# Optimization experiments

Hardware: AMD Instinct MI355X
Metric: run time of the kernel (lower is better)

The kernel has to match this reference:

```python
import jax, jax.numpy as jnp
import numpy as np

B, S, D = 4, 2048, 1024
H, HD = 16, 64            # num heads, head dim (H*HD == D)
FF = 4096                  # llama intermediate size
EPS = 1e-6
THETA = 10000.0


def rms_norm(x, w):
    v = jnp.mean(jnp.square(x), axis=-1, keepdims=True)
    return x * jax.lax.rsqrt(v + EPS) * w


def apply_rope(x, pos):
    # x: [B,H,S,HD]; HF llama rotate_half convention
    inv = 1.0 / (THETA ** (jnp.arange(0, HD, 2, dtype=jnp.float32) / HD))  # [HD/2]
    ang = pos[:, None].astype(jnp.float32) * inv[None, :]                   # [S,HD/2]
    cos = jnp.concatenate([jnp.cos(ang), jnp.cos(ang)], -1)[None, None]     # [1,1,S,HD]
    sin = jnp.concatenate([jnp.sin(ang), jnp.sin(ang)], -1)[None, None]
    x1, x2 = jnp.split(x, 2, axis=-1)
    return x * cos + jnp.concatenate([-x2, x1], axis=-1) * sin


def setup_inputs() -> dict:
    key = jax.random.key(0)
    ks = jax.random.split(key, 12)
    p = lambda k, shp: (0.02 * jax.random.normal(k, shp, dtype=jnp.float32))
    return {
        "chunk_hidden_states": jax.random.normal(ks[0], (B, S, D), dtype=jnp.float32),
        "Wq": p(ks[1], (D, D)),
        "Wk": p(ks[2], (D, D)),
        "Wv": p(ks[3], (D, D)),
        "Wo": p(ks[4], (D, D)),
        "ln1_w": jnp.ones((D,), dtype=jnp.float32),
        "ln2_w": jnp.ones((D,), dtype=jnp.float32),
        "Wgate": p(ks[5], (FF, D)),
        "Wup": p(ks[6], (FF, D)),
        "Wdown": p(ks[7], (D, FF)),
        "W_out": p(ks[8], (1024, D)),
        "b_out": jnp.zeros((1024,), dtype=jnp.float32),
    }


def reference(chunk_hidden_states, Wq, Wk, Wv, Wo, ln1_w, ln2_w,
              Wgate, Wup, Wdown, W_out, b_out):
    x = chunk_hidden_states                      # [B,S,D]
    pos = jnp.arange(S)

    # --- self attention block ---
    h = rms_norm(x, ln1_w)
    q = (h @ Wq.T).reshape(B, S, H, HD).transpose(0, 2, 1, 3)  # [B,H,S,HD]
    k = (h @ Wk.T).reshape(B, S, H, HD).transpose(0, 2, 1, 3)
    v = (h @ Wv.T).reshape(B, S, H, HD).transpose(0, 2, 1, 3)
    q = apply_rope(q, pos)
    k = apply_rope(k, pos)
    # attention_mask is None when the layer is called directly -> full (non-causal) attention
    scores = jnp.einsum("bhqd,bhkd->bhqk", q, k) / jnp.sqrt(jnp.float32(HD))
    attn = jax.nn.softmax(scores, axis=-1)
    ctx = jnp.einsum("bhqk,bhkd->bhqd", attn, v)             # [B,H,S,HD]
    ctx = ctx.transpose(0, 2, 1, 3).reshape(B, S, D)
    x = x + ctx @ Wo.T

    # --- MLP block (SwiGLU) ---
    h2 = rms_norm(x, ln2_w)
    mlp = (jax.nn.silu(h2 @ Wgate.T) * (h2 @ Wup.T)) @ Wdown.T
    x = x + mlp

    # --- output head ---
    logits = x @ W_out.T + b_out                 # [B,S,1024]
    return logits.reshape(-1, 8, 1024)
```

## Files before the change

### kernel.cpp

```cpp
#include <hip/hip_runtime.h>

#define TB 4
#define TS 2048
#define TD 1024
#define TH 16
#define THD 64
#define TFF 4096
#define TTOK (TB*TS)

typedef unsigned int  uint32;
typedef unsigned short u16;
typedef short s8v __attribute__((ext_vector_type(8)));
typedef short s4bf __attribute__((ext_vector_type(4)));
typedef float f4v __attribute__((ext_vector_type(4)));

#define BF16_MAGIC 0x3f803f80u

__device__ __forceinline__ u16 f2bf(float f){
    uint32 u = __float_as_uint(f);
    u += 0x7fffu + ((u >> 16) & 1u);
    return (u16)(u >> 16);
}
__device__ __forceinline__ float bf2f(u16 h){
    return __uint_as_float(((uint32)h) << 16);
}
__device__ __forceinline__ void gload_lds16(const void* g, void* l){
    __builtin_amdgcn_global_load_lds(
        (const __attribute__((address_space(1))) unsigned int*)g,
        (__attribute__((address_space(3))) unsigned int*)l,
        16, 0, 0);
}

struct CvtDesc { const void* src; void* dst; int n; int mode; };
struct CvtArgs { CvtDesc d[13]; };

__global__ __launch_bounds__(256)
void cvt_all(CvtArgs a, const uint32* __restrict__ flag){
    const bool isbf = (*flag == BF16_MAGIC);
    CvtDesc dd = a.d[blockIdx.y];
    if (dd.mode == 2){
        float* cosT = (float*)dd.dst;
        float* sinT = cosT + TS*32;
        for (int i = blockIdx.x*256 + threadIdx.x; i < dd.n; i += 256*gridDim.x){
            int s = i >> 5, f = i & 31;
            double inv = pow(10000.0, -(double)f/32.0);
            double ang = (double)s * inv;
            cosT[i] = (float)cos(ang);
            sinT[i] = (float)sin(ang);
        }
        return;
    }
    int n4 = dd.n >> 2;
    if (dd.mode == 1){
        float* dst = (float*)dd.dst;
        for (int i = blockIdx.x*256 + threadIdx.x; i < n4; i += 256*gridDim.x){
            float4 v;
            if (isbf){
                ushort4 u = ((const ushort4*)dd.src)[i];
                v = make_float4(bf2f(u.x), bf2f(u.y), bf2f(u.z), bf2f(u.w));
            } else v = ((const float4*)dd.src)[i];
            ((float4*)dst)[i] = v;
        }
        return;
    }
    for (int i = blockIdx.x*256 + threadIdx.x; i < n4; i += 256*gridDim.x){
        ushort4 o;
        if (isbf) o = ((const ushort4*)dd.src)[i];
        else {
            float4 v = ((const float4*)dd.src)[i];
            o.x=f2bf(v.x); o.y=f2bf(v.y); o.z=f2bf(v.z); o.w=f2bf(v.w);
        }
        size_t di = i;
        if (dd.mode >= 3){
            int row = i >> 8, c4 = i & 255;
            int drow = ((row >> 6) << 7) + (row & 63) + ((dd.mode == 4) ? 64 : 0);
            di = (size_t)drow*256 + c4;
        }
        ((ushort4*)dd.dst)[di] = o;
    }
}

__global__ __launch_bounds__(256)
void rmsnorm_k(const float* __restrict__ x, const float* __restrict__ w, u16* __restrict__ out){
    int row = blockIdx.x, tid = threadIdx.x;
    float4 xv = ((const float4*)(x + (size_t)row*TD))[tid];
    float s = xv.x*xv.x + xv.y*xv.y + xv.z*xv.z + xv.w*xv.w;
    #pragma unroll
    for (int off = 32; off > 0; off >>= 1) s += __shfl_xor(s, off);
    __shared__ float red[4];
    if ((tid & 63) == 0) red[tid >> 6] = s;
    __syncthreads();
    float tot = red[0]+red[1]+red[2]+red[3];
    float rs = rsqrtf(tot * (1.0f/TD) + 1e-6f);
    float4 wv = ((const float4*)w)[tid];
    ushort4 o;
    o.x = f2bf(xv.x*rs*wv.x); o.y = f2bf(xv.y*rs*wv.y);
    o.z = f2bf(xv.z*rs*wv.z); o.w = f2bf(xv.w*rs*wv.w);
    ((ushort4*)(out + (size_t)row*TD))[tid] = o;
}

enum { EPI_ADDF32 = 1, EPI_OUT = 3, EPI_QKVROPE = 4, EPI_ADDBF16 = 5, EPI_GATEUP = 6 };

template<int EPI>
__global__ __launch_bounds__(256)
void gemm_bt(const u16* __restrict__ A, int lda,
             const u16* __restrict__ W, int ldw,
             int K,
             void* __restrict__ outp, int ldo,
             const float* __restrict__ bias,
             const uint32* __restrict__ flag,
             u16* __restrict__ q_out, u16* __restrict__ k_out, u16* __restrict__ vt_out,
             const float* __restrict__ cosT, const float* __restrict__ sinT,
             const float* __restrict__ resid)
{
    __shared__ __align__(16) u16 SMEM[2*128*64];
    u16* As = SMEM;
    u16* Bs = SMEM + 128*64;
    const int tid  = threadIdx.x;
    const int wave = tid >> 6;
    const int lane = tid & 63;
    const int tm = blockIdx.y * 128;
    const int tn = blockIdx.x * 128;
    const int wm = (wave >> 1) * 64;
    const int wn = (wave &  1) * 64;

    f4v acc[4][4] = {};

    const int srow8 = lane >> 3;
    const int ch    = lane & 7;
    const int lrow  = lane & 15;
    const int lq    = lane >> 4;

    const u16* Ag = A + (size_t)(tm + wave*32 + srow8)*lda + ((ch ^ srow8) << 3);
    const u16* Wg = W + (size_t)(tn + wave*32 + srow8)*ldw + ((ch ^ srow8) << 3);

    for (int k0 = 0; k0 < K; k0 += 64){
        __syncthreads();
        #pragma unroll
        for (int i8 = 0; i8 < 4; i8++){
            gload_lds16(Ag + (size_t)(i8*8)*lda + k0, As + (wave*32 + i8*8)*64);
            gload_lds16(Wg + (size_t)(i8*8)*ldw + k0, Bs + (wave*32 + i8*8)*64);
        }
        __syncthreads();

        #pragma unroll
        for (int kk = 0; kk < 2; kk++){
            s8v a[4], b[4];
            #pragma unroll
            for (int i = 0; i < 4; i++){
                int row = wm + i*16 + lrow;
                a[i] = *(const s8v*)(As + row*64 + (((kk*4 + lq) ^ (lrow & 7)) << 3));
            }
            #pragma unroll
            for (int j = 0; j < 4; j++){
                int row = wn + j*16 + lrow;
                b[j] = *(const s8v*)(Bs + row*64 + (((kk*4 + lq) ^ (lrow & 7)) << 3));
            }
            #pragma unroll
            for (int i = 0; i < 4; i++)
                #pragma unroll
                for (int j = 0; j < 4; j++)
                    acc[i][j] = __builtin_amdgcn_mfma_f32_16x16x32_bf16(a[i], b[j], acc[i][j], 0, 0, 0);
        }
    }

    if constexpr (EPI == EPI_QKVROPE){
        const int ncol0 = tn + wn;
        if (ncol0 < 2048){
            u16* dst = (ncol0 < 1024) ? q_out : k_out;
            const int cbase = ncol0 & 1023;
            #pragma unroll
            for (int i = 0; i < 4; i++){
                #pragma unroll
                for (int r = 0; r < 4; r++){
                    int row = tm + wm + i*16 + lq*4 + r;
                    int s = row & (TS-1);
                    #pragma unroll
                    for (int j = 0; j < 2; j++){
                        int d = j*16 + lrow;
                        float c  = cosT[s*32 + d];
                        float sn = sinT[s*32 + d];
                        float x1 = acc[i][j][r], x2 = acc[i][j+2][r];
                        dst[(size_t)row*TD + cbase + d]      = f2bf(x1*c - x2*sn);
                        dst[(size_t)row*TD + cbase + d + 32] = f2bf(x2*c + x1*sn);
                    }
                }
            }
        } else {
            #pragma unroll
            for (int i = 0; i < 4; i++)
                #pragma unroll
                for (int j = 0; j < 4; j++)
                    #pragma unroll
                    for (int r = 0; r < 4; r++){
                        int row = tm + wm + i*16 + lq*4 + r;
                        int col = ncol0 - 2048 + j*16 + lrow;
                        int bb = row >> 11, s = row & (TS-1);
                        int hh = col >> 6, hd = col & 63;
                        vt_out[((size_t)(bb*TH + hh)*THD + hd)*TS + s] = f2bf(acc[i][j][r]);
                    }
        }
        return;
    }

    if constexpr (EPI == EPI_GATEUP){
        __syncthreads();
        float* upL = (float*)SMEM;
        const int widx = wave >> 1;
        if (wave & 1){
            #pragma unroll
            for (int i = 0; i < 4; i++)
                #pragma unroll
                for (int j = 0; j < 4; j++)
                    #pragma unroll
                    for (int r = 0; r < 4; r++)
                        upL[widx*4096 + (i*16 + lq*4 + r)*64 + j*16 + lrow] = acc[i][j][r];
        }
        __syncthreads();
        if (!(wave & 1)){
            #pragma unroll
            for (int i = 0; i < 4; i++)
                #pragma unroll
                for (int j = 0; j < 4; j++)
                    #pragma unroll
                    for (int r = 0; r < 4; r++){
                        float g = acc[i][j][r];
                        float u = upL[widx*4096 + (i*16 + lq*4 + r)*64 + j*16 + lrow];
                        float mres = (g / (1.0f + __expf(-g))) * u;
                        int row = tm + wm + i*16 + lq*4 + r;
                        int fcol = blockIdx.x*64 + j*16 + lrow;
                        ((u16*)outp)[(size_t)row*TFF + fcol] = f2bf(mres);
                    }
        }
        return;
    }

    bool obf = false;
    if (EPI == EPI_OUT) obf = (*flag == BF16_MAGIC);
    #pragma unroll
    for (int i = 0; i < 4; i++){
        #pragma unroll
        for (int j = 0; j < 4; j++){
            #pragma unroll
            for (int r = 0; r < 4; r++){
                int row = tm + wm + i*16 + lq*4 + r;
                int col = tn + wn + j*16 + lrow;
                size_t idx = (size_t)row*ldo + col;
                float val = acc[i][j][r];
                if constexpr (EPI == EPI_ADDF32){
                    float* o = (float*)outp;
                    o[idx] += val;
                } else if constexpr (EPI == EPI_ADDBF16){
                    ((u16*)outp)[idx] = f2bf(resid[idx] + val);
                } else {
                    float v2 = val + bias[col];
                    if (obf) ((u16*)outp)[idx] = f2bf(v2);
                    else     ((float*)outp)[idx] = v2;
                }
            }
        }
    }
}

__global__ __launch_bounds__(256, 2)
void flash_attn_mfma(const u16* __restrict__ qg, const u16* __restrict__ kg,
                     const u16* __restrict__ vt, u16* __restrict__ ctx)
{
    __shared__ u16 Qs[128*64];
    __shared__ u16 Ks[64*64];
    __shared__ u16 VT2[8*64*8];
    const int tid  = threadIdx.x;
    const int wave = tid >> 6;
    const int lane = tid & 63;
    const int qd   = lane >> 4;
    const int mm   = lane & 15;
    const int b  = blockIdx.y >> 4, h = blockIdx.y & 15;
    const int q0 = blockIdx.x * 128;
    const size_t tok0 = (size_t)b * TS;
    const u16* vtb = vt + (size_t)(b*TH + h)*THD*TS;
    const int rl = lane >> 3, ch = lane & 7;

    #pragma unroll
    for (int i = 0; i < 4; i++){
        int row = wave*32 + i*8 + rl;
        const u16* gp = qg + (tok0 + q0 + row)*TD + h*THD + ((ch ^ (row & 7)) << 3);
        gload_lds16(gp, Qs + (wave*32 + i*8)*64);
    }
    __syncthreads();

    s8v qf[2][2];
    #pragma unroll
    for (int ct = 0; ct < 2; ct++){
        int row = wave*32 + ct*16 + mm;
        #pragma unroll
        for (int hs = 0; hs < 2; hs++)
            qf[ct][hs] = *(const s8v*)(Qs + row*64 + (((hs*4 + qd) ^ (row & 7)) << 3));
    }

    f4v acc[2][4] = {};
    float mrun[2] = {-3.0e38f, -3.0e38f};
    float lrun[2] = {0.0f, 0.0f};
    const float SC2 = 0.18033688011112042f;

    for (int kt = 0; kt < TS/64; kt++){
        __syncthreads();
        #pragma unroll
        for (int i = 0; i < 2; i++){
            int row = wave*16 + i*8 + rl;
            const u16* gp = kg + (tok0 + kt*64 + row)*TD + h*THD + ((ch ^ (row & 7)) << 3);
            gload_lds16(gp, Ks + (wave*16 + i*8)*64);
        }
        #pragma unroll
        for (int ii = 0; ii < 2; ii++){
            int kb = wave*2 + ii;
            const u16* gp = vtb + (size_t)lane*TS + kt*64 + kb*8;
            gload_lds16(gp, VT2 + kb*64*8);
        }
        __syncthreads();

        f4v sc[4][2] = {};
        #pragma unroll
        for (int rt = 0; rt < 4; rt++){
            int row = rt*16 + mm;
            #pragma unroll
            for (int hs = 0; hs < 2; hs++){
                s8v kf = *(const s8v*)(Ks + row*64 + (((hs*4 + qd) ^ (row & 7)) << 3));
                #pragma unroll
                for (int ct = 0; ct < 2; ct++)
                    sc[rt][ct] = __builtin_amdgcn_mfma_f32_16x16x32_bf16(kf, qf[ct][hs], sc[rt][ct], 0, 0, 0);
            }
        }
        union VU { s4bf h[2]; s8v v; };
        VU vf8[2][4];
        #pragma unroll
        for (int t = 0; t < 2; t++){
            int kbA = 4*t + (qd >> 1);
            #pragma unroll
            for (int n = 0; n < 4; n++){
                const u16* base = VT2 + ((16*n + mm)*8) + ((qd & 1) * 4);
                vf8[t][n].h[0] = *(const s4bf*)(base + kbA*512);
                vf8[t][n].h[1] = *(const s4bf*)(base + (kbA+2)*512);
            }
        }

        #pragma unroll
        for (int ct = 0; ct < 2; ct++){
            float mx = sc[0][ct][0];
            #pragma unroll
            for (int rt = 0; rt < 4; rt++)
                #pragma unroll
                for (int r = 0; r < 4; r++)
                    mx = fmaxf(mx, sc[rt][ct][r]);
            mx = fmaxf(mx, __shfl_xor(mx, 16));
            mx = fmaxf(mx, __shfl_xor(mx, 32));
            float mn = fmaxf(mrun[ct], mx * SC2);
            float alpha = __builtin_amdgcn_exp2f(mrun[ct] - mn);
            mrun[ct] = mn;
            float ls = 0.0f;
            uint32 pk[4][2];
            #pragma unroll
            for (int rt = 0; rt < 4; rt++){
                float p0 = __builtin_amdgcn_exp2f(fmaf(sc[rt][ct][0], SC2, -mn));
                float p1 = __builtin_amdgcn_exp2f(fmaf(sc[rt][ct][1], SC2, -mn));
                float p2 = __builtin_amdgcn_exp2f(fmaf(sc[rt][ct][2], SC2, -mn));
                float p3 = __builtin_amdgcn_exp2f(fmaf(sc[rt][ct][3], SC2, -mn));
                ls += (p0 + p1) + (p2 + p3);
                pk[rt][0] = (__float_as_uint(p0) >> 16) | (__float_as_uint(p1) & 0xFFFF0000u);
                pk[rt][1] = (__float_as_uint(p2) >> 16) | (__float_as_uint(p3) & 0xFFFF0000u);
            }
            ls += __shfl_xor(ls, 16);
            ls += __shfl_xor(ls, 32);
            lrun[ct] = lrun[ct]*alpha + ls;
            #pragma unroll
            for (int r = 0; r < 4; r++){
                float ar = __shfl(alpha, (lane & 48) + qd*4 + r);
                #pragma unroll
                for (int n = 0; n < 4; n++)
                    acc[ct][n][r] *= ar;
            }
            #pragma unroll
            for (int t = 0; t < 2; t++){
                union { uint32 u[4]; s8v s; } pu;
                pu.u[0] = pk[2*t][0];   pu.u[1] = pk[2*t][1];
                pu.u[2] = pk[2*t+1][0]; pu.u[3] = pk[2*t+1][1];
                #pragma unroll
                for (int n = 0; n < 4; n++)
                    acc[ct][n] = __builtin_amdgcn_mfma_f32_16x16x32_bf16(pu.s, vf8[t][n].v, acc[ct][n], 0, 0, 0);
            }
        }
    }
    #pragma unroll
    for (int ct = 0; ct < 2; ct++){
        float rli = 1.0f / lrun[ct];
        #pragma unroll
        for (int r = 0; r < 4; r++){
            float ir = __shfl(rli, (lane & 48) + qd*4 + r);
            int row = q0 + wave*32 + ct*16 + qd*4 + r;
            u16* op = ctx + (tok0 + row)*TD + h*THD + mm;
            #pragma unroll
            for (int n = 0; n < 4; n++)
                op[16*n] = f2bf(acc[ct][n][r] * ir);
        }
    }
}

extern "C" void kernel_launch(void* const* d_in, const int* in_sizes, int n_in,
                              void* d_out, int out_size, void* d_ws, size_t ws_size,
                              hipStream_t stream)
{
    const uint32* flag = (const uint32*)d_in[5];
    char* ws = (char*)d_ws;
    size_t off = 0;
    auto alloc = [&](size_t bytes) -> void* {
        void* p = ws + off;
        off += (bytes + 255) & ~(size_t)255;
        return p;
    };
    float* xf   = (float*)alloc((size_t)TTOK*TD*4);
    u16*   hbf  = (u16*)  alloc((size_t)TTOK*TD*2);
    u16*   qb   = (u16*)  alloc((size_t)TTOK*TD*2);
    u16*   kb   = (u16*)  alloc((size_t)TTOK*TD*2);
    u16*   cb   = (u16*)  alloc((size_t)TTOK*TD*2);
    u16*   vt   = (u16*)  alloc((size_t)TTOK*TD*2);
    u16*   wqkv = (u16*)  alloc((size_t)3*TD*TD*2);
    u16*   wo   = (u16*)  alloc((size_t)TD*TD*2);
    u16*   wfu  = (u16*)  alloc((size_t)2*TFF*TD*2);
    u16*   wd   = (u16*)  alloc((size_t)TD*TFF*2);
    u16*   wou  = (u16*)  alloc((size_t)TD*TD*2);
    float* ln1  = (float*)alloc(TD*4);
    float* ln2  = (float*)alloc(TD*4);
    float* bo   = (float*)alloc(TD*4);
    float* cosT = (float*)alloc((size_t)TS*32*4*2);
    float* sinT = cosT + TS*32;
    u16*   mbuf = qb;
    (void)ws_size; (void)in_sizes; (void)n_in; (void)out_size;

    CvtArgs ca;
    ca.d[0]  = { d_in[0],  xf,            TTOK*TD, 1 };
    ca.d[1]  = { d_in[1],  wqkv,          TD*TD,   0 };
    ca.d[2]  = { d_in[2],  wqkv + (size_t)TD*TD,   TD*TD, 0 };
    ca.d[3]  = { d_in[3],  wqkv + (size_t)2*TD*TD, TD*TD, 0 };
    ca.d[4]  = { d_in[4],  wo,            TD*TD,   0 };
    ca.d[5]  = { d_in[7],  wfu,           TFF*TD,  3 };
    ca.d[6]  = { d_in[8],  wfu,           TFF*TD,  4 };
    ca.d[7]  = { d_in[9],  wd,            TD*TFF,  0 };
    ca.d[8]  = { d_in[10], wou,           TD*TD,   0 };
    ca.d[9]  = { d_in[5],  ln1,           TD,      1 };
    ca.d[10] = { d_in[6],  ln2,           TD,      1 };
    ca.d[11] = { d_in[11], bo,            TD,      1 };
    ca.d[12] = { nullptr,  cosT,          TS*32,   2 };
    cvt_all<<<dim3(256,13),256,0,stream>>>(ca, flag);

    rmsnorm_k<<<TTOK,256,0,stream>>>(xf, ln1, hbf);
    gemm_bt<EPI_QKVROPE><<<dim3(24, TTOK/128),256,0,stream>>>(
        hbf, TD, wqkv, TD, TD, nullptr, 0, nullptr, nullptr,
        qb, kb, vt, cosT, sinT, nullptr);
    flash_attn_mfma<<<dim3(TS/128, TB*TH),256,0,stream>>>(qb, kb, vt, cb);
    gemm_bt<EPI_ADDF32><<<dim3(TD/128, TTOK/128),256,0,stream>>>(
        cb, TD, wo, TD, TD, xf, TD, nullptr, nullptr,
        nullptr, nullptr, nullptr, nullptr, nullptr, nullptr);

    rmsnorm_k<<<TTOK,256,0,stream>>>(xf, ln2, hbf);
    gemm_bt<EPI_GATEUP><<<dim3(2*TFF/128, TTOK/128),256,0,stream>>>(
        hbf, TD, wfu, TD, TD, mbuf, TFF, nullptr, nullptr,
        nullptr, nullptr, nullptr, nullptr, nullptr, nullptr);
    gemm_bt<EPI_ADDBF16><<<dim3(TD/128, TTOK/128),256,0,stream>>>(
        mbuf, TFF, wd, TFF, TFF, hbf, TD, nullptr, nullptr,
        nullptr, nullptr, nullptr, nullptr, nullptr, xf);

    gemm_bt<EPI_OUT><<<dim3(TD/128, TTOK/128),256,0,stream>>>(
        hbf, TD, wou, TD, TD, d_out, TD, bo, flag,
        nullptr, nullptr, nullptr, nullptr, nullptr, nullptr);
}
```

Measured before the change: 716.1 us.

## Add 256x256 double-buffered GEMM for MLP and swizzle block order

Adds a 512-thread gemm256 kernel with 256x256 tiles, double-buffered LDS staging and interleaved sub-tile loads and MFMAs with manual barriers and vmcnt waits. It replaces the 128-tile gate/up and down-projection GEMMs, raising operand reuse and overlapping global loads with compute. Block indices in the existing GEMM and flash attention kernels are also remapped for better L2 locality. The hand-written waitcnt schedule is fragile, and the larger tiles give fewer blocks per CU.

```diff
diff --git a/kernel.cpp b/kernel.cpp
--- a/kernel.cpp
+++ b/kernel.cpp
@@ -30,6 +30,14 @@
         (__attribute__((address_space(3))) unsigned int*)l,
         16, 0, 0);
 }
+__device__ __forceinline__ void bar(){
+    asm volatile("" ::: "memory");
+    __builtin_amdgcn_s_barrier();
+    asm volatile("" ::: "memory");
+}
+#define WAITVM4() asm volatile("s_waitcnt vmcnt(4)" ::: "memory")
+#define WAITVM2() asm volatile("s_waitcnt vmcnt(2)" ::: "memory")
+#define WAITVM0() asm volatile("s_waitcnt vmcnt(0)" ::: "memory")
 
 struct CvtDesc { const void* src; void* dst; int n; int mode; };
 struct CvtArgs { CvtDesc d[13]; };
@@ -119,8 +127,11 @@
     const int tid  = threadIdx.x;
     const int wave = tid >> 6;
     const int lane = tid & 63;
-    const int tm = blockIdx.y * 128;
-    const int tn = blockIdx.x * 128;
+    const int nbx = gridDim.x;
+    const int lin = blockIdx.y * nbx + blockIdx.x;
+    const int swz = (lin & 7) * ((nbx * gridDim.y) >> 3) + (lin >> 3);
+    const int tm = (swz / nbx) * 128;
+    const int tn = (swz % nbx) * 128;
     const int wm = (wave >> 1) * 64;
     const int wn = (wave &  1) * 64;
 
@@ -198,38 +209,6 @@
                         int bb = row >> 11, s = row & (TS-1);
                         int hh = col >> 6, hd = col & 63;
                         vt_out[((size_t)(bb*TH + hh)*THD + hd)*TS + s] = f2bf(acc[i][j][r]);
-                    }
-        }
-        return;
-    }
-
-    if constexpr (EPI == EPI_GATEUP){
-        __syncthreads();
-        float* upL = (float*)SMEM;
-        const int widx = wave >> 1;
-        if (wave & 1){
-            #pragma unroll
-            for (int i = 0; i < 4; i++)
-                #pragma unroll
-                for (int j = 0; j < 4; j++)
-                    #pragma unroll
-                    for (int r = 0; r < 4; r++)
-                        upL[widx*4096 + (i*16 + lq*4 + r)*64 + j*16 + lrow] = acc[i][j][r];
-        }
-        __syncthreads();
-        if (!(wave & 1)){
-            #pragma unroll
-            for (int i = 0; i < 4; i++)
-                #pragma unroll
-                for (int j = 0; j < 4; j++)
-                    #pragma unroll
-                    for (int r = 0; r < 4; r++){
-                        float g = acc[i][j][r];
-                        float u = upL[widx*4096 + (i*16 + lq*4 + r)*64 + j*16 + lrow];
-                        float mres = (g / (1.0f + __expf(-g))) * u;
-                        int row = tm + wm + i*16 + lq*4 + r;
-                        int fcol = blockIdx.x*64 + j*16 + lrow;
-                        ((u16*)outp)[(size_t)row*TFF + fcol] = f2bf(mres);
                     }
         }
         return;
@@ -262,6 +241,191 @@
     }
 }
 
+template<int EPI>
+__global__ __launch_bounds__(512, 2)
+void gemm256(const u16* __restrict__ A, int lda,
+             const u16* __restrict__ W, int ldw,
+             int K,
+             void* __restrict__ outp, int ldo,
+             const float* __restrict__ resid)
+{
+    __shared__ __align__(16) u16 SM[2][2*256*64];
+    const int tid  = threadIdx.x;
+    const int wave = tid >> 6;
+    const int lane = tid & 63;
+    const int wm = wave >> 2;
+    const int wn = wave & 3;
+    const int lrow = lane & 15;
+    const int lq   = lane >> 4;
+    const int srow8 = lane >> 3;
+    const int ch    = lane & 7;
+
+    const int nbx = gridDim.x;
+    const int lin = blockIdx.y * nbx + blockIdx.x;
+    const int swz = (lin & 7) * ((nbx * gridDim.y) >> 3) + (lin >> 3);
+    const int tm = (swz / nbx) * 256;
+    const int tn = (swz % nbx) * 256;
+
+    const int NT = K >> 6;
+
+    const u16* Ag = A + (size_t)(tm + wave*8 + srow8)*lda + ((ch ^ srow8) << 3);
+    const u16* Wg = W + (size_t)(tn + wave*8 + srow8)*ldw + ((ch ^ srow8) << 3);
+
+    f4v acc[2][4][2][2] = {};
+    s8v a[2][4];
+    s8v b[2][2][2];
+
+    auto stageA = [&](int bufi, int g, int t){
+        size_t k0 = (size_t)t * 64;
+        #pragma unroll
+        for (int r = 0; r < 2; r++)
+            gload_lds16(Ag + (size_t)(g*128 + r*64)*lda + k0,
+                        &SM[bufi][(g*128 + r*64 + wave*8)*64]);
+    };
+    auto stageB = [&](int bufi, int h, int t){
+        size_t k0 = (size_t)t * 64;
+        #pragma unroll
+        for (int r = 0; r < 2; r++)
+            gload_lds16(Wg + (size_t)(h*128 + r*64)*ldw + k0,
+                        &SM[bufi][256*64 + (h*128 + r*64 + wave*8)*64]);
+    };
+    auto ldA = [&](int bufi, int g){
+        #pragma unroll
+        for (int kk = 0; kk < 2; kk++)
+            #pragma unroll
+            for (int i = 0; i < 4; i++){
+                int row = g*128 + wm*64 + i*16 + lrow;
+                a[kk][i] = *(const s8v*)(&SM[bufi][row*64 + (((kk*4 + lq) ^ (lrow & 7)) << 3)]);
+            }
+    };
+    auto ldB = [&](int bufi, int h){
+        #pragma unroll
+        for (int kk = 0; kk < 2; kk++)
+            #pragma unroll
+            for (int j = 0; j < 2; j++){
+                int row = h*128 + wn*32 + j*16 + lrow;
+                b[h][kk][j] = *(const s8v*)(&SM[bufi][256*64 + row*64 + (((kk*4 + lq) ^ (lrow & 7)) << 3)]);
+            }
+    };
+    auto mmac = [&](int g, int h){
+        __builtin_amdgcn_s_setprio(1);
+        #pragma unroll
+        for (int kk = 0; kk < 2; kk++)
+            #pragma unroll
+            for (int i = 0; i < 4; i++)
+                #pragma unroll
+                for (int j = 0; j < 2; j++)
+                    acc[g][i][h][j] = __builtin_amdgcn_mfma_f32_16x16x32_bf16(
+                        a[kk][i], b[h][kk][j], acc[g][i][h][j], 0, 0, 0);
+        __builtin_amdgcn_s_setprio(0);
+    };
+
+    stageA(0,0,0); stageB(0,0,0); stageB(0,1,0); stageA(0,1,0);
+    WAITVM4(); bar();
+
+    for (int t = 0; t < NT-1; t++){
+        const int buf = t & 1, nb = buf ^ 1;
+        ldA(buf,0); ldB(buf,0);
+        stageA(nb,0,t+1);
+        bar();
+        mmac(0,0);
+        WAITVM4(); bar();
+        ldB(buf,1);
+        stageB(nb,0,t+1);
+        bar();
+        mmac(0,1);
+        WAITVM4(); bar();
+        ldA(buf,1);
+        stageB(nb,1,t+1);
+        bar();
+        mmac(1,0);
+        bar();
+        stageA(nb,1,t+1);
+        bar();
+        mmac(1,1);
+        WAITVM4(); bar();
+    }
+    {
+        const int buf = (NT-1) & 1;
+        ldA(buf,0); ldB(buf,0);
+        bar();
+        mmac(0,0);
+        WAITVM2(); bar();
+        ldB(buf,1);
+        bar();
+        mmac(0,1);
+        WAITVM0(); bar();
+        ldA(buf,1);
+        bar();
+        mmac(1,0);
+        bar();
+        mmac(1,1);
+    }
+
+    if constexpr (EPI == EPI_GATEUP){
+        bar();
+        float* X = (float*)&SM[0][0];
+        const int uw = wm*2 + (wn & 1);
+        if (wn >= 2){
+            #pragma unroll
+            for (int g = 0; g < 2; g++)
+            #pragma unroll
+            for (int i = 0; i < 4; i++)
+            #pragma unroll
+            for (int h = 0; h < 2; h++)
+            #pragma unroll
+            for (int j = 0; j < 2; j++)
+            #pragma unroll
+            for (int r = 0; r < 4; r++)
+                X[uw*8192 + (g*64 + i*16 + lq*4 + r)*64
+                          + ((h*32 + j*16 + lrow) ^ (lq << 3))] = acc[g][i][h][j][r];
+        }
+        bar();
+        if (wn < 2){
+            u16* o = (u16*)outp;
+            #pragma unroll
+            for (int g = 0; g < 2; g++)
+            #pragma unroll
+            for (int i = 0; i < 4; i++)
+            #pragma unroll
+            for (int h = 0; h < 2; h++)
+            #pragma unroll
+            for (int j = 0; j < 2; j++)
+            #pragma unroll
+            for (int r = 0; r < 4; r++){
+                float gv = acc[g][i][h][j][r];
+                float uv = X[uw*8192 + (g*64 + i*16 + lq*4 + r)*64
+                                     + ((h*32 + j*16 + lrow) ^ (lq << 3))];
+                float mres = (gv / (1.0f + __expf(-gv))) * uv;
+                int row = tm + g*128 + wm*64 + i*16 + lq*4 + r;
+                int ff  = (tn >> 1) + h*64 + wn*32 + j*16 + lrow;
+                o[(size_t)row*TFF + ff] = f2bf(mres);
+            }
+        }
+        return;
+    }
+
+    if constexpr (EPI == EPI_ADDBF16){
+        u16* o = (u16*)outp;
+        #pragma unroll
+        for (int g = 0; g < 2; g++)
+        #pragma unroll
+        for (int i = 0; i < 4; i++)
+        #pragma unroll
+        for (int h = 0; h < 2; h++)
+        #pragma unroll
+        for (int j = 0; j < 2; j++)
+        #pragma unroll
+        for (int r = 0; r < 4; r++){
+            int row = tm + g*128 + wm*64 + i*16 + lq*4 + r;
+            int col = tn + h*128 + wn*32 + j*16 + lrow;
+            size_t idx = (size_t)row*ldo + col;
+            o[idx] = f2bf(resid[idx] + acc[g][i][h][j][r]);
+        }
+        return;
+    }
+}
+
 __global__ __launch_bounds__(256, 2)
 void flash_attn_mfma(const u16* __restrict__ qg, const u16* __restrict__ kg,
                      const u16* __restrict__ vt, u16* __restrict__ ctx)
@@ -274,8 +438,10 @@
     const int lane = tid & 63;
     const int qd   = lane >> 4;
     const int mm   = lane & 15;
-    const int b  = blockIdx.y >> 4, h = blockIdx.y & 15;
-    const int q0 = blockIdx.x * 128;
+    const int lin = blockIdx.y * 16 + blockIdx.x;
+    const int swz = (lin & 7) * 128 + (lin >> 3);
+    const int b  = swz >> 8, h = (swz >> 4) & 15;
+    const int q0 = (swz & 15) * 128;
     const size_t tok0 = (size_t)b * TS;
     const u16* vtb = vt + (size_t)(b*TH + h)*THD*TS;
     const int rl = lane >> 3, ch = lane & 7;
@@ -461,12 +627,10 @@
         nullptr, nullptr, nullptr, nullptr, nullptr, nullptr);
 
     rmsnorm_k<<<TTOK,256,0,stream>>>(xf, ln2, hbf);
-    gemm_bt<EPI_GATEUP><<<dim3(2*TFF/128, TTOK/128),256,0,stream>>>(
-        hbf, TD, wfu, TD, TD, mbuf, TFF, nullptr, nullptr,
-        nullptr, nullptr, nullptr, nullptr, nullptr, nullptr);
-    gemm_bt<EPI_ADDBF16><<<dim3(TD/128, TTOK/128),256,0,stream>>>(
-        mbuf, TFF, wd, TFF, TFF, hbf, TD, nullptr, nullptr,
-        nullptr, nullptr, nullptr, nullptr, nullptr, xf);
+    gemm256<EPI_GATEUP><<<dim3(2*TFF/256, TTOK/256),512,0,stream>>>(
+        hbf, TD, wfu, TD, TD, mbuf, TFF, nullptr);
+    gemm256<EPI_ADDBF16><<<dim3(TD/256, TTOK/256),512,0,stream>>>(
+        mbuf, TFF, wd, TFF, TFF, hbf, TD, xf);
 
     gemm_bt<EPI_OUT><<<dim3(TD/128, TTOK/128),256,0,stream>>>(
         hbf, TD, wou, TD, TD, d_out, TD, bo, flag,
```

After: 701.2 us. -2.1%, faster.
